# Kernel tuning notes

Hardware: AMD Instinct MI355X
Metric: run time of the kernel (lower is better)

## Reference

```python
import jax, jax.numpy as jnp
import numpy as np

N_NODES = 100000
N_EDGES = 1000000
NHID = 128
N_CLASSES = 5000


def setup_inputs() -> dict:
    key = jax.random.key(0)
    ks = jax.random.split(key, 8)
    feature = jax.random.normal(ks[0], (N_NODES, NHID), dtype=jnp.float32)
    # Linear weights stored as [in, out] so forward is x @ W + b
    W1 = jax.random.normal(ks[1], (2 * NHID, NHID), dtype=jnp.float32) * (1.0 / np.sqrt(2 * NHID))
    b1 = jnp.zeros((NHID,), dtype=jnp.float32)
    alpha = jnp.full((NHID,), 0.25, dtype=jnp.float32)  # PReLU per-channel init
    W2 = jax.random.normal(ks[2], (NHID, 2), dtype=jnp.float32) * (1.0 / np.sqrt(NHID))
    b2 = jnp.zeros((2,), dtype=jnp.float32)
    row = jax.random.randint(ks[3], (N_EDGES,), 0, N_NODES, dtype=jnp.int64)
    col = jax.random.randint(ks[4], (N_EDGES,), 0, N_NODES, dtype=jnp.int64)
    label = jax.random.randint(ks[5], (N_NODES,), 0, N_CLASSES, dtype=jnp.int64)
    return {"feature": feature, "W1": W1, "b1": b1, "alpha": alpha,
            "W2": W2, "b2": b2, "row": row, "col": col, "label": label}


def reference(feature, W1, b1, alpha, W2, b2, row, col, label):
    # per-edge label: 1 if endpoints share a cluster label
    y = (label[row] == label[col]).astype(jnp.int32)  # [E]
    # edge gather + concat: [E, 2*nhid]
    x = jnp.concatenate([feature[row], feature[col]], axis=1)
    h = x @ W1 + b1                                   # [E, nhid]
    h = jnp.where(h >= 0, h, alpha * h)               # PReLU, per-channel alpha
    logits = h @ W2 + b2                              # [E, 2]
    logp = jax.nn.log_softmax(logits, axis=-1)
    # mean cross-entropy over edges
    loss = -jnp.mean(jnp.take_along_axis(logp, y[:, None], axis=1))
    return loss
```

## Files before the change

kernel.cpp:

```cpp
#include <hip/hip_runtime.h>
#include <hip/hip_bf16.h>

typedef __bf16 bf16_t;
typedef bf16_t bf16x8 __attribute__((ext_vector_type(8)));
typedef float floatx4 __attribute__((ext_vector_type(4)));

#define N_NODES 100000
#define N_EDGES 1000000
#define NHID 128
#define PQ_COLS 256

__global__ __launch_bounds__(256) void k_prep(const float* __restrict__ W1,
                                              const float* __restrict__ alpha,
                                              const float* __restrict__ W2,
                                              const float* __restrict__ b2,
                                              bf16_t* __restrict__ WT,
                                              float* __restrict__ wdp,
                                              float* __restrict__ wdn,
                                              float* __restrict__ dbias) {
    int i = blockIdx.x * 256 + threadIdx.x;
    int n = i >> 7;
    int k = i & 127;
    float v = (n < 128) ? W1[k * 128 + n] : W1[(k + 128) * 128 + (n - 128)];
    WT[i] = (bf16_t)v;
    if (blockIdx.x == 0) {
        if (threadIdx.x < 128) {
            float wd = W2[threadIdx.x * 2 + 1] - W2[threadIdx.x * 2 + 0];
            wdp[threadIdx.x] = wd;
            wdn[threadIdx.x] = wd * alpha[threadIdx.x];
        } else if (threadIdx.x == 128) {
            *dbias = b2[1] - b2[0];
        }
    }
}

__global__ __launch_bounds__(256) void k_gemm_pq(const float* __restrict__ F,
                                                 const bf16_t* __restrict__ WT,
                                                 const float* __restrict__ b1,
                                                 bf16_t* __restrict__ PQ) {
    __shared__ bf16x8 As8[1024];
    const int t = threadIdx.x;
    const int m0 = blockIdx.x * 64;

#pragma unroll
    for (int j = 0; j < 8; ++j) {
        int chunk = j * 256 + t;
        int r = chunk >> 5;
        int c4 = chunk & 31;
        int gr = m0 + r;
        float4 u = {0.f, 0.f, 0.f, 0.f};
        if (gr < N_NODES) u = ((const float4*)F)[(size_t)gr * 32 + c4];
        int s    = c4 >> 3;
        int quad = (c4 >> 1) & 3;
        int half = c4 & 1;
        bf16_t* dst = (bf16_t*)&As8[(((r >> 4) * 4 + s) * 4 + quad) * 16 + (r & 15)] + half * 4;
        dst[0] = (bf16_t)u.x; dst[1] = (bf16_t)u.y; dst[2] = (bf16_t)u.z; dst[3] = (bf16_t)u.w;
    }
    __syncthreads();

    const int wave = t >> 6, lane = t & 63;
    const int l15 = lane & 15, quad = lane >> 4;
    const int n0 = wave * 64;

    float bias_v[4];
#pragma unroll
    for (int nt = 0; nt < 4; ++nt) {
        int n = n0 + nt * 16 + l15;
        bias_v[nt] = (n < 128) ? b1[n] : 0.f;
    }

    floatx4 acc[4][4] = {};
#pragma unroll
    for (int s = 0; s < 4; ++s) {
        bf16x8 a[4], b[4];
#pragma unroll
        for (int mt = 0; mt < 4; ++mt)
            a[mt] = As8[(mt * 4 + s) * 64 + lane];
#pragma unroll
        for (int nt = 0; nt < 4; ++nt)
            b[nt] = *(const bf16x8*)(WT + (size_t)(n0 + nt * 16 + l15) * NHID + s * 32 + quad * 8);
#pragma unroll
        for (int mt = 0; mt < 4; ++mt)
#pragma unroll
            for (int nt = 0; nt < 4; ++nt)
                acc[mt][nt] = __builtin_amdgcn_mfma_f32_16x16x32_bf16(a[mt], b[nt], acc[mt][nt], 0, 0, 0);
    }

    bf16_t* Tb = (bf16_t*)As8;
#pragma unroll
    for (int h = 0; h < 2; ++h) {
        __syncthreads();
#pragma unroll
        for (int mi = 0; mi < 2; ++mi) {
            int mt = h * 2 + mi;
#pragma unroll
            for (int r = 0; r < 4; ++r) {
                int rl = mi * 16 + quad * 4 + r;
                int sw = ((rl >> 2) & 3) << 4;
#pragma unroll
                for (int nt = 0; nt < 4; ++nt) {
                    int col = n0 + nt * 16 + l15;
                    Tb[rl * 256 + (col ^ sw)] = (bf16_t)(acc[mt][nt][r] + bias_v[nt]);
                }
            }
        }
        __syncthreads();
#pragma unroll
        for (int j = 0; j < 4; ++j) {
            int chunk = j * 256 + t;
            int rl  = chunk >> 5;
            int c16 = chunk & 31;
            int grow = m0 + h * 32 + rl;
            if (grow < N_NODES) {
                bf16x8 v = ((bf16x8*)Tb)[rl * 32 + (c16 ^ ((rl >> 2) & 3) * 2)];
                ((bf16x8*)(PQ + (size_t)grow * PQ_COLS))[c16] = v;
            }
        }
    }
}

__global__ __launch_bounds__(256) void k_edge_loss(const bf16_t* __restrict__ PQ,
                                                   const float* __restrict__ wdp_g,
                                                   const float* __restrict__ wdn_g,
                                                   const float* __restrict__ dbias_g,
                                                   const int* __restrict__ row,
                                                   const int* __restrict__ col,
                                                   const int* __restrict__ label,
                                                   float* __restrict__ out) {
    const int lg = threadIdx.x & 15;
    const int group = (blockIdx.x * blockDim.x + threadIdx.x) >> 4;
    const int ng = (gridDim.x * blockDim.x) >> 4;
    const int ch = lg * 8;

    float wdp[8], wdn[8];
#pragma unroll
    for (int j = 0; j < 8; ++j) { wdp[j] = wdp_g[ch + j]; wdn[j] = wdn_g[ch + j]; }
    const float dbias = *dbias_g;

    float acc = 0.f;
    for (int e = group; e < N_EDGES; e += 4 * ng) {
        int ei[4]; bool vl[4];
#pragma unroll
        for (int k = 0; k < 4; ++k) {
            int ee = e + k * ng;
            vl[k] = (ee < N_EDGES);
            ei[k] = vl[k] ? ee : e;
        }
        int r[4], c[4];
#pragma unroll
        for (int k = 0; k < 4; ++k) { r[k] = row[ei[k]]; c[k] = col[ei[k]]; }
        bf16x8 p[4], q[4];
#pragma unroll
        for (int k = 0; k < 4; ++k) {
            p[k] = *(const bf16x8*)(PQ + (size_t)r[k] * PQ_COLS + ch);
            q[k] = *(const bf16x8*)(PQ + (size_t)c[k] * PQ_COLS + 128 + ch);
        }
        int yr[4], yc[4];
#pragma unroll
        for (int k = 0; k < 4; ++k) { yr[k] = label[r[k]]; yc[k] = label[c[k]]; }

        float d[4] = {0.f, 0.f, 0.f, 0.f};
#pragma unroll
        for (int j = 0; j < 8; ++j) {
#pragma unroll
            for (int k = 0; k < 4; ++k) {
                float h = (float)p[k][j] + (float)q[k][j];
                d[k] = fmaf(h, (h >= 0.f) ? wdp[j] : wdn[j], d[k]);
            }
        }
#pragma unroll
        for (int m = 8; m >= 1; m >>= 1) {
#pragma unroll
            for (int k = 0; k < 4; ++k) d[k] += __shfl_xor(d[k], m, 16);
        }
        if (lg == 0) {
#pragma unroll
            for (int k = 0; k < 4; ++k) {
                float D = d[k] + dbias;
                float s = (yr[k] == yc[k]) ? -D : D;
                float loss = fmaxf(s, 0.f) + log1pf(expf(-fabsf(s)));
                if (vl[k]) acc += loss;
            }
        }
    }
#pragma unroll
    for (int m = 32; m >= 1; m >>= 1) acc += __shfl_xor(acc, m, 64);
    __shared__ float sdata[4];
    int lane = threadIdx.x & 63;
    int wv = threadIdx.x >> 6;
    if (lane == 0) sdata[wv] = acc;
    __syncthreads();
    if (threadIdx.x == 0) {
        float s = (sdata[0] + sdata[1]) + (sdata[2] + sdata[3]);
        atomicAdd(out, s * (1.f / (float)N_EDGES));
    }
}

extern "C" void kernel_launch(void* const* d_in, const int* in_sizes, int n_in,
                              void* d_out, int out_size, void* d_ws, size_t ws_size,
                              hipStream_t stream) {
    const float* feature = (const float*)d_in[0];
    const float* W1      = (const float*)d_in[1];
    const float* b1      = (const float*)d_in[2];
    const float* alpha   = (const float*)d_in[3];
    const float* W2      = (const float*)d_in[4];
    const float* b2      = (const float*)d_in[5];
    const int*   row     = (const int*)d_in[6];
    const int*   col     = (const int*)d_in[7];
    const int*   label   = (const int*)d_in[8];
    float* out = (float*)d_out;

    char* ws = (char*)d_ws;
    bf16_t* PQ   = (bf16_t*)(ws);
    bf16_t* WT   = (bf16_t*)(ws + 51200000);
    float*  wdp  = (float*)(ws + 51265536);
    float*  wdn  = (float*)(ws + 51266048);
    float*  dbias= (float*)(ws + 51266560);

    hipMemsetAsync(d_out, 0, sizeof(float), stream);

    k_prep<<<128, 256, 0, stream>>>(W1, alpha, W2, b2, WT, wdp, wdn, dbias);
    k_gemm_pq<<<1563, 256, 0, stream>>>(feature, WT, b1, PQ);
    k_edge_loss<<<2048, 256, 0, stream>>>(PQ, wdp, wdn, dbias, row, col, label, out);
}
```

Baseline: 212.4 us.

## Split PReLU into linear plus abs term, store PQ in fp8, precompute per-node linear part

```diff
diff --git a/kernel.cpp b/kernel.cpp
--- a/kernel.cpp
+++ b/kernel.cpp
@@ -4,6 +4,7 @@
 typedef __bf16 bf16_t;
 typedef bf16_t bf16x8 __attribute__((ext_vector_type(8)));
 typedef float floatx4 __attribute__((ext_vector_type(4)));
+typedef float floatx2 __attribute__((ext_vector_type(2)));
 
 #define N_NODES 100000
 #define N_EDGES 1000000
@@ -11,25 +12,45 @@
 #define PQ_COLS 256
 
 __global__ __launch_bounds__(256) void k_prep(const float* __restrict__ W1,
+                                              const float* __restrict__ b1,
                                               const float* __restrict__ alpha,
                                               const float* __restrict__ W2,
                                               const float* __restrict__ b2,
                                               bf16_t* __restrict__ WT,
-                                              float* __restrict__ wdp,
-                                              float* __restrict__ wdn,
-                                              float* __restrict__ dbias) {
+                                              float* __restrict__ wabsg,
+                                              float* __restrict__ u1g,
+                                              float* __restrict__ u2g,
+                                              float* __restrict__ constg) {
+    __shared__ float w1L[128];
     int i = blockIdx.x * 256 + threadIdx.x;
-    int n = i >> 7;
-    int k = i & 127;
-    float v = (n < 128) ? W1[k * 128 + n] : W1[(k + 128) * 128 + (n - 128)];
-    WT[i] = (bf16_t)v;
-    if (blockIdx.x == 0) {
-        if (threadIdx.x < 128) {
-            float wd = W2[threadIdx.x * 2 + 1] - W2[threadIdx.x * 2 + 0];
-            wdp[threadIdx.x] = wd;
-            wdn[threadIdx.x] = wd * alpha[threadIdx.x];
-        } else if (threadIdx.x == 128) {
-            *dbias = b2[1] - b2[0];
+    if (i < 32768) {
+        int n = i >> 7;
+        int k = i & 127;
+        float v = (n < 128) ? W1[k * 128 + n] : W1[(k + 128) * 128 + (n - 128)];
+        WT[i] = (bf16_t)v;
+    }
+    if (blockIdx.x == 128) {
+        int t = threadIdx.x;
+        if (t < 128) {
+            float wd = W2[2 * t + 1] - W2[2 * t];
+            float al = alpha[t];
+            w1L[t] = wd * (1.f + al) * 0.5f;
+            wabsg[t] = wd * (1.f - al) * 0.5f;
+        }
+        __syncthreads();
+        if (t < 128) {
+            float a1 = 0.f, a2 = 0.f;
+            for (int j = 0; j < 128; ++j) {
+                a1 = fmaf(W1[t * 128 + j], w1L[j], a1);
+                a2 = fmaf(W1[(t + 128) * 128 + j], w1L[j], a2);
+            }
+            u1g[t] = a1;
+            u2g[t] = a2;
+        }
+        if (t == 0) {
+            float c = 0.f;
+            for (int j = 0; j < 128; ++j) c = fmaf(w1L[j], b1[j], c);
+            *constg = c + (b2[1] - b2[0]);
         }
     }
 }
@@ -37,8 +58,14 @@
 __global__ __launch_bounds__(256) void k_gemm_pq(const float* __restrict__ F,
                                                  const bf16_t* __restrict__ WT,
                                                  const float* __restrict__ b1,
-                                                 bf16_t* __restrict__ PQ) {
+                                                 const float* __restrict__ u1g,
+                                                 const float* __restrict__ u2g,
+                                                 const int* __restrict__ label,
+                                                 unsigned char* __restrict__ PQ8,
+                                                 float4* __restrict__ aux_g) {
     __shared__ bf16x8 As8[1024];
+    __shared__ float sp1[4][64];
+    __shared__ float sp2[4][64];
     const int t = threadIdx.x;
     const int m0 = blockIdx.x * 64;
 
@@ -86,6 +113,35 @@
                 acc[mt][nt] = __builtin_amdgcn_mfma_f32_16x16x32_bf16(a[mt], b[nt], acc[mt][nt], 0, 0, 0);
     }
 
+    {
+        int rr = t & 63, part = t >> 6;
+        int mt_ = rr >> 4, r15 = rr & 15;
+        float a1 = 0.f, a2 = 0.f;
+#pragma unroll
+        for (int qd = 0; qd < 4; ++qd) {
+            bf16x8 av = As8[((mt_ * 4 + part) * 4 + qd) * 16 + r15];
+#pragma unroll
+            for (int idx = 0; idx < 8; ++idx) {
+                float fv = (float)av[idx];
+                int kk = part * 32 + qd * 8 + idx;
+                a1 = fmaf(fv, u1g[kk], a1);
+                a2 = fmaf(fv, u2g[kk], a2);
+            }
+        }
+        sp1[part][rr] = a1;
+        sp2[part][rr] = a2;
+    }
+    __syncthreads();
+    if (t < 64) {
+        int grow = m0 + t;
+        if (grow < N_NODES) {
+            float s1 = (sp1[0][t] + sp1[1][t]) + (sp1[2][t] + sp1[3][t]);
+            float s2 = (sp2[0][t] + sp2[1][t]) + (sp2[2][t] + sp2[3][t]);
+            float4 av = {s1, s2, __int_as_float(label[grow]), 0.f};
+            aux_g[grow] = av;
+        }
+    }
+
     bf16_t* Tb = (bf16_t*)As8;
 #pragma unroll
     for (int h = 0; h < 2; ++h) {
@@ -99,8 +155,8 @@
                 int sw = ((rl >> 2) & 3) << 4;
 #pragma unroll
                 for (int nt = 0; nt < 4; ++nt) {
-                    int col = n0 + nt * 16 + l15;
-                    Tb[rl * 256 + (col ^ sw)] = (bf16_t)(acc[mt][nt][r] + bias_v[nt]);
+                    int colx = n0 + nt * 16 + l15;
+                    Tb[rl * 256 + (colx ^ sw)] = (bf16_t)(acc[mt][nt][r] + bias_v[nt]);
                 }
             }
         }
@@ -113,29 +169,34 @@
             int grow = m0 + h * 32 + rl;
             if (grow < N_NODES) {
                 bf16x8 v = ((bf16x8*)Tb)[rl * 32 + (c16 ^ ((rl >> 2) & 3) * 2)];
-                ((bf16x8*)(PQ + (size_t)grow * PQ_COLS))[c16] = v;
+                unsigned int lo = 0, hi = 0;
+                lo = __builtin_amdgcn_cvt_pk_fp8_f32((float)v[0], (float)v[1], lo, false);
+                lo = __builtin_amdgcn_cvt_pk_fp8_f32((float)v[2], (float)v[3], lo, true);
+                hi = __builtin_amdgcn_cvt_pk_fp8_f32((float)v[4], (float)v[5], hi, false);
+                hi = __builtin_amdgcn_cvt_pk_fp8_f32((float)v[6], (float)v[7], hi, true);
+                uint2 pk; pk.x = lo; pk.y = hi;
+                ((uint2*)(PQ8 + (size_t)grow * PQ_COLS))[c16] = pk;
             }
         }
     }
 }
 
-__global__ __launch_bounds__(256) void k_edge_loss(const bf16_t* __restrict__ PQ,
-                                                   const float* __restrict__ wdp_g,
-                                                   const float* __restrict__ wdn_g,
-                                                   const float* __restrict__ dbias_g,
+__global__ __launch_bounds__(256) void k_edge_loss(const unsigned char* __restrict__ PQ8,
+                                                   const float4* __restrict__ aux,
+                                                   const float* __restrict__ wabsg,
+                                                   const float* __restrict__ constg,
                                                    const int* __restrict__ row,
                                                    const int* __restrict__ col,
-                                                   const int* __restrict__ label,
                                                    float* __restrict__ out) {
     const int lg = threadIdx.x & 15;
     const int group = (blockIdx.x * blockDim.x + threadIdx.x) >> 4;
     const int ng = (gridDim.x * blockDim.x) >> 4;
     const int ch = lg * 8;
 
-    float wdp[8], wdn[8];
-#pragma unroll
-    for (int j = 0; j < 8; ++j) { wdp[j] = wdp_g[ch + j]; wdn[j] = wdn_g[ch + j]; }
-    const float dbias = *dbias_g;
+    float wabs[8];
+#pragma unroll
+    for (int j = 0; j < 8; ++j) wabs[j] = wabsg[ch + j];
+    const float CB = *constg;
 
     float acc = 0.f;
     for (int e = group; e < N_EDGES; e += 4 * ng) {
@@ -149,36 +210,52 @@
         int r[4], c[4];
 #pragma unroll
         for (int k = 0; k < 4; ++k) { r[k] = row[ei[k]]; c[k] = col[ei[k]]; }
-        bf16x8 p[4], q[4];
+        uint2 p[4], q[4];
 #pragma unroll
         for (int k = 0; k < 4; ++k) {
-            p[k] = *(const bf16x8*)(PQ + (size_t)r[k] * PQ_COLS + ch);
-            q[k] = *(const bf16x8*)(PQ + (size_t)c[k] * PQ_COLS + 128 + ch);
-        }
-        int yr[4], yc[4];
-#pragma unroll
-        for (int k = 0; k < 4; ++k) { yr[k] = label[r[k]]; yc[k] = label[c[k]]; }
-
-        float d[4] = {0.f, 0.f, 0.f, 0.f};
-#pragma unroll
-        for (int j = 0; j < 8; ++j) {
+            p[k] = *(const uint2*)(PQ8 + (size_t)r[k] * PQ_COLS + ch);
+            q[k] = *(const uint2*)(PQ8 + (size_t)c[k] * PQ_COLS + 128 + ch);
+        }
+
+        float sab[4] = {0.f, 0.f, 0.f, 0.f};
+#pragma unroll
+        for (int k = 0; k < 4; ++k) {
+            floatx2 p01 = __builtin_amdgcn_cvt_pk_f32_fp8((int)p[k].x, false);
+            floatx2 p23 = __builtin_amdgcn_cvt_pk_f32_fp8((int)p[k].x, true);
+            floatx2 p45 = __builtin_amdgcn_cvt_pk_f32_fp8((int)p[k].y, false);
+            floatx2 p67 = __builtin_amdgcn_cvt_pk_f32_fp8((int)p[k].y, true);
+            floatx2 q01 = __builtin_amdgcn_cvt_pk_f32_fp8((int)q[k].x, false);
+            floatx2 q23 = __builtin_amdgcn_cvt_pk_f32_fp8((int)q[k].x, true);
+            floatx2 q45 = __builtin_amdgcn_cvt_pk_f32_fp8((int)q[k].y, false);
+            floatx2 q67 = __builtin_amdgcn_cvt_pk_f32_fp8((int)q[k].y, true);
+            floatx2 h01 = p01 + q01;
+            floatx2 h23 = p23 + q23;
+            floatx2 h45 = p45 + q45;
+            floatx2 h67 = p67 + q67;
+            float s = sab[k];
+            s = fmaf(fabsf(h01[0]), wabs[0], s);
+            s = fmaf(fabsf(h01[1]), wabs[1], s);
+            s = fmaf(fabsf(h23[0]), wabs[2], s);
+            s = fmaf(fabsf(h23[1]), wabs[3], s);
+            s = fmaf(fabsf(h45[0]), wabs[4], s);
+            s = fmaf(fabsf(h45[1]), wabs[5], s);
+            s = fmaf(fabsf(h67[0]), wabs[6], s);
+            s = fmaf(fabsf(h67[1]), wabs[7], s);
+            sab[k] = s;
+        }
+#pragma unroll
+        for (int m = 8; m >= 1; m >>= 1) {
+#pragma unroll
+            for (int k = 0; k < 4; ++k) sab[k] += __shfl_xor(sab[k], m, 16);
+        }
+        if (lg == 0) {
 #pragma unroll
             for (int k = 0; k < 4; ++k) {
-                float h = (float)p[k][j] + (float)q[k][j];
-                d[k] = fmaf(h, (h >= 0.f) ? wdp[j] : wdn[j], d[k]);
-            }
-        }
-#pragma unroll
-        for (int m = 8; m >= 1; m >>= 1) {
-#pragma unroll
-            for (int k = 0; k < 4; ++k) d[k] += __shfl_xor(d[k], m, 16);
-        }
-        if (lg == 0) {
-#pragma unroll
-            for (int k = 0; k < 4; ++k) {
-                float D = d[k] + dbias;
-                float s = (yr[k] == yc[k]) ? -D : D;
-                float loss = fmaxf(s, 0.f) + log1pf(expf(-fabsf(s)));
+                float4 ar = aux[r[k]];
+                float4 ac2 = aux[c[k]];
+                float D = ar.x + ac2.y + CB + sab[k];
+                float s = (__float_as_int(ar.z) == __float_as_int(ac2.z)) ? -D : D;
+                float loss = fmaxf(s, 0.f) + __logf(1.f + __expf(-fabsf(s)));
                 if (vl[k]) acc += loss;
             }
         }
@@ -211,15 +288,17 @@
     float* out = (float*)d_out;
 
     char* ws = (char*)d_ws;
-    bf16_t* PQ   = (bf16_t*)(ws);
-    bf16_t* WT   = (bf16_t*)(ws + 51200000);
-    float*  wdp  = (float*)(ws + 51265536);
-    float*  wdn  = (float*)(ws + 51266048);
-    float*  dbias= (float*)(ws + 51266560);
+    unsigned char* PQ8 = (unsigned char*)(ws);
+    float4* aux  = (float4*)(ws + 25600000);
+    bf16_t* WT   = (bf16_t*)(ws + 27200000);
+    float* wabsg = (float*)(ws + 27265536);
+    float* u1g   = (float*)(ws + 27266048);
+    float* u2g   = (float*)(ws + 27266560);
+    float* constg= (float*)(ws + 27267072);
 
     hipMemsetAsync(d_out, 0, sizeof(float), stream);
 
-    k_prep<<<128, 256, 0, stream>>>(W1, alpha, W2, b2, WT, wdp, wdn, dbias);
-    k_gemm_pq<<<1563, 256, 0, stream>>>(feature, WT, b1, PQ);
-    k_edge_loss<<<2048, 256, 0, stream>>>(PQ, wdp, wdn, dbias, row, col, label, out);
+    k_prep<<<129, 256, 0, stream>>>(W1, b1, alpha, W2, b2, WT, wabsg, u1g, u2g, constg);
+    k_gemm_pq<<<1563, 256, 0, stream>>>(feature, WT, b1, u1g, u2g, label, PQ8, aux);
+    k_edge_loss<<<4096, 256, 0, stream>>>(PQ8, aux, wabsg, constg, row, col, out);
 }
```

After: 210.3 us. No clear change (-1.0%).
